# Performance work log

Hardware: AMD Instinct MI355X
Metric: run time of the kernel (lower is better)

Reference implementation:

```python
import jax, jax.numpy as jnp
import numpy as np

B, N, P, D = 256, 196, 768, 768
FIXED_MASK = 40          # FIXED_MASK_COUNT in the TF source
FIXED_UNMASK = N - FIXED_MASK


def setup_inputs() -> dict:
    key = jax.random.key(0)
    k1, k2, k3, k4, k5 = jax.random.split(key, 5)
    return {
        "patches": jax.random.normal(k1, (B, N, P), jnp.float32),
        "rand_u": jax.random.uniform(k2, (B, N), jnp.float32),
        "W": jax.random.normal(k3, (P, D), jnp.float32) * 0.02,
        "b": jnp.zeros((D,), jnp.float32),
        "pos_table": jax.random.normal(k4, (N, D), jnp.float32) * 0.02,
        "mask_token": jax.random.normal(k5, (1, P), jnp.float32),
    }


def reference(patches, rand_u, W, b, pos_table, mask_token):
    Bsz, Np, _ = patches.shape
    pos = pos_table[None]                                   # [1,N,D]
    patch_emb = jnp.einsum("bnp,pd->bnd", patches, W) + b + pos  # [B,N,D]

    # ---- get_smart_indices ----
    patch_means = jnp.mean(jnp.abs(patches), axis=2)        # [B,N]
    valid_mask = (patch_means > 0).astype(jnp.float32)
    valid_counts = jnp.sum(valid_mask, axis=1)
    max_masks = jnp.ceil(valid_counts * 0.4).astype(jnp.int32)
    valid_image = (valid_counts >= 20) & (max_masks >= FIXED_MASK)  # [B]

    # scores: valid patches in [1000,2000), invalid in [0,10)
    scores = valid_mask * (1000.0 + 1000.0 * rand_u) + (1.0 - valid_mask) * (10.0 * rand_u)
    _, top_idx = jax.lax.top_k(scores, FIXED_MASK)          # first 40 of full top-k sort
    top_idx = top_idx.astype(jnp.int32)
    mask_indices = jnp.where(valid_image[:, None], top_idx, jnp.zeros_like(top_idx))
    mask_counts = jnp.where(valid_image, FIXED_MASK, 0).astype(jnp.int32)

    # complement (ascending order), vectorized stream compaction via sort key
    flag = jnp.zeros((Bsz, Np), jnp.int32).at[jnp.arange(Bsz)[:, None], mask_indices].set(1)
    sort_key = flag * Np + jnp.arange(Np, dtype=jnp.int32)[None]  # unmasked sort first, ascending
    comp = jnp.argsort(sort_key, axis=1)[:, :FIXED_UNMASK].astype(jnp.int32)
    unmask_indices = jnp.where(valid_image[:, None], comp,
                               jnp.arange(FIXED_UNMASK, dtype=jnp.int32)[None])

    # ---- batched gathers ----
    pos_b = jnp.broadcast_to(pos, patch_emb.shape)          # [B,N,D]
    take = lambda x, i: jnp.take_along_axis(x, i[..., None], axis=1)
    unmasked_embeddings = take(patch_emb, unmask_indices)   # [B,156,D]
    unmasked_positions = take(pos_b, unmask_indices)        # [B,156,D]
    masked_positions = take(pos_b, mask_indices)            # [B,40,D]

    mtok = mask_token @ W + b                               # [1,D]
    masked_embeddings = mtok[None] + masked_positions       # [B,40,D]

    # validity masking (counts are 40 for valid images, 0 otherwise)
    seq = jnp.arange(FIXED_MASK, dtype=jnp.int32)[None]
    validity = (seq < mask_counts[:, None]).astype(jnp.float32)[..., None]
    masked_embeddings = masked_embeddings * validity

    return (unmasked_embeddings, masked_embeddings, unmasked_positions,
            mask_indices, unmask_indices)
```

## Files before the change

kernel.cpp:

```cpp
#include <hip/hip_runtime.h>
#include <hip/hip_bf16.h>
#include <stdint.h>

#define BATCH 256
#define NP    196
#define PP    768
#define DD    768
#define FM    40
#define FU    156
#define ROWS  39936

#define O_UE 0ull
#define O_ME 30670848ull
#define O_UP 38535168ull
#define O_MI 69206016ull
#define O_UI 69216256ull

typedef __attribute__((ext_vector_type(8))) short short8;
typedef __attribute__((ext_vector_type(4))) float f32x4;

__device__ __forceinline__ unsigned short bf16_rne(float x) {
    unsigned u = __float_as_uint(x);
    u += 0x7FFFu + ((u >> 16) & 1u);
    return (unsigned short)(u >> 16);
}
__device__ __forceinline__ float bf16_f(unsigned short h) {
    return __uint_as_float(((unsigned)h) << 16);
}

__device__ __forceinline__ void gl_lds16(const void* gsrc, void* ldst) {
    __builtin_amdgcn_global_load_lds(
        (const __attribute__((address_space(1))) unsigned*)gsrc,
        (__attribute__((address_space(3))) unsigned*)ldst, 16, 0, 0);
}

__global__ __launch_bounds__(256) void prep_w_kernel(
    const float* __restrict__ W,
    unsigned short* __restrict__ wt) {
    const int j  = blockIdx.x * 256 + threadIdx.x;
    const int ct = blockIdx.y;
    const int kt = blockIdx.z;
    const int row  = j >> 2;
    const int slot = j & 3;
    const int g    = slot ^ ((row >> 1) & 3);
    const int d    = ct * 128 + row;
    alignas(16) unsigned short hi[8];
    alignas(16) unsigned short lo[8];
#pragma unroll
    for (int e = 0; e < 8; ++e) {
        int k32 = (e < 4) ? (4 * g + e) : (12 + 4 * g + e);
        float x = W[(size_t)(kt * 32 + k32) * DD + d];
        unsigned short h = bf16_rne(x);
        hi[e] = h;
        lo[e] = bf16_rne(x - bf16_f(h));
    }
    unsigned short* dst = wt + ((size_t)(kt * 6 + ct) * 1024 + j) * 8;
    *(uint4*)dst          = *(const uint4*)hi;
    *(uint4*)(dst + 4096) = *(const uint4*)lo;
}

__global__ __launch_bounds__(256) void mtok_part_kernel(
    const float* __restrict__ mask_token,
    const float* __restrict__ W,
    float* __restrict__ part) {
    const int j = blockIdx.x;
    const int tid = threadIdx.x;
#pragma unroll
    for (int s = 0; s < 3; ++s) {
        int d = tid + s * 256;
        float acc = 0.f;
        for (int p = j * 64; p < j * 64 + 64; ++p)
            acc += mask_token[p] * W[(size_t)p * DD + d];
        part[(size_t)j * DD + d] = acc;
    }
}
__global__ __launch_bounds__(256) void mtok_red_kernel(
    const float* __restrict__ part,
    const float* __restrict__ bias,
    float* __restrict__ mtok_out) {
    int d = blockIdx.x * 256 + threadIdx.x;
    float acc = bias[d];
#pragma unroll
    for (int j = 0; j < 12; ++j) acc += part[(size_t)j * DD + d];
    mtok_out[d] = acc;
}

__global__ __launch_bounds__(256) void select_kernel(
    const float* __restrict__ patches,
    const float* __restrict__ rand_u,
    float* __restrict__ out,
    int* __restrict__ gidx,
    int* __restrict__ pidx,
    int* __restrict__ midx,
    int* __restrict__ valid_arr) {

    const int b = blockIdx.x;
    const int tid = threadIdx.x;
    __shared__ unsigned long long key[256];
    __shared__ int s_flag[256];
    __shared__ int s_scan[256];
    __shared__ int wsum[4];

    int v = 0;
    if (tid < NP) {
        const float* row = patches + ((size_t)b * NP + tid) * PP;
        for (int p = 0; p < PP; ++p) {
            if (row[p] != 0.0f) { v = 1; break; }
        }
    }
    unsigned long long bal = __ballot(v != 0);
    if ((tid & 63) == 0) wsum[tid >> 6] = __popcll(bal);
    __syncthreads();
    int count = wsum[0] + wsum[1] + wsum[2] + wsum[3];
    bool valid_image = (count >= 20) && (ceilf((float)count * 0.4f) >= 40.0f);

    unsigned long long k = 0ull;
    if (tid < NP) {
        float u = rand_u[(size_t)b * NP + tid];
        float score = v ? __fadd_rn(1000.0f, __fmul_rn(1000.0f, u))
                        : __fmul_rn(10.0f, u);
        k = (((unsigned long long)__float_as_uint(score)) << 32) |
            (unsigned long long)(unsigned)(~tid);
    }
    key[tid] = k;
    __syncthreads();

    for (int kk = 2; kk <= 256; kk <<= 1) {
        for (int j = kk >> 1; j > 0; j >>= 1) {
            int ixj = tid ^ j;
            if (ixj > tid) {
                unsigned long long a = key[tid], c = key[ixj];
                bool desc = ((tid & kk) == 0);
                if (desc ? (a < c) : (a > c)) { key[tid] = c; key[ixj] = a; }
            }
            __syncthreads();
        }
    }

    int m_out = 0;
    if (tid < FM) {
        int idx = (int)(~(unsigned)(key[tid] & 0xFFFFFFFFull));
        m_out = valid_image ? idx : 0;
        midx[b * FM + tid] = m_out;
        out[O_MI + (size_t)b * FM + tid] = (float)m_out;
    }
    s_flag[tid] = 0;
    __syncthreads();
    if (tid < FM) s_flag[m_out] = 1;
    __syncthreads();

    int x = (tid < NP) ? (1 - s_flag[tid]) : 0;
    s_scan[tid] = x;
    __syncthreads();
    for (int off = 1; off < 256; off <<= 1) {
        int t2 = (tid >= off) ? s_scan[tid - off] : 0;
        __syncthreads();
        s_scan[tid] += t2;
        __syncthreads();
    }
    int pos = s_scan[tid] - x;

    if (valid_image) {
        if (tid < NP && !s_flag[tid] && pos < FU) {
            gidx[(size_t)b * FU + pos] = b * NP + tid;
            pidx[(size_t)b * FU + pos] = tid;
            out[O_UI + (size_t)b * FU + pos] = (float)tid;
        }
    } else {
        if (tid < FU) {
            gidx[(size_t)b * FU + tid] = b * NP + tid;
            pidx[(size_t)b * FU + tid] = tid;
            out[O_UI + (size_t)b * FU + tid] = (float)tid;
        }
    }
    if (tid == 0) valid_arr[b] = valid_image ? 1 : 0;
}

__global__ __launch_bounds__(192) void prep_p_kernel(
    const float* __restrict__ patches,
    const int* __restrict__ gidx,
    char* __restrict__ pat_bf) {
    const int r = blockIdx.x;
    const int t = threadIdx.x;
    const float* src = patches + (size_t)gidx[r] * PP;
    float4 v4 = *(const float4*)(src + 4 * t);
    const int kt = t >> 3;
    const int q  = t & 7;
    const int g  = q & 3;
    const int half = q >> 2;
    float vs[4] = {v4.x, v4.y, v4.z, v4.w};
    unsigned long long hp = 0, lp = 0;
#pragma unroll
    for (int e = 0; e < 4; ++e) {
        unsigned short h = bf16_rne(vs[e]);
        unsigned short l = bf16_rne(vs[e] - bf16_f(h));
        hp |= ((unsigned long long)h) << (16 * e);
        lp |= ((unsigned long long)l) << (16 * e);
    }
    char* dst = pat_bf + (size_t)r * 3072 + kt * 64 + g * 16 + half * 8;
    *(unsigned long long*)dst          = hp;
    *(unsigned long long*)(dst + 1536) = lp;
}

template <int PRE>
__device__ __forceinline__ void fetchB(int KT, short8 (&BH)[4], short8 (&BL)[4],
                                       const char* const (&pb)[4],
                                       const float* const (&prow)[4], int g) {
    if constexpr (PRE) {
#pragma unroll
        for (int ci = 0; ci < 4; ++ci) {
            const char* p = pb[ci] + KT * 64;
            BH[ci] = *(const short8*)p;
            BL[ci] = *(const short8*)(p + 1536);
        }
    } else {
#pragma unroll
        for (int ci = 0; ci < 4; ++ci) {
            const float* p = prow[ci] + KT * 32 + 4 * g;
            const float4 a  = *(const float4*)p;
            const float4 b2 = *(const float4*)(p + 16);
            float vs[8] = {a.x, a.y, a.z, a.w, b2.x, b2.y, b2.z, b2.w};
            short8 h8, l8;
#pragma unroll
            for (int e = 0; e < 8; ++e) {
                unsigned short h = bf16_rne(vs[e]);
                h8[e] = (short)h;
                l8[e] = (short)bf16_rne(vs[e] - bf16_f(h));
            }
            BH[ci] = h8;
            BL[ci] = l8;
        }
    }
}

template <int PRE>
__global__ __launch_bounds__(256) void gemm_kernel(
    const float* __restrict__ patches,
    const char* __restrict__ pat_bf,
    const unsigned short* __restrict__ wt,
    const float* __restrict__ bias,
    const float* __restrict__ pos_table,
    const int* __restrict__ gidx,
    const int* __restrict__ pidx,
    float* __restrict__ out) {

    __shared__ __align__(16) char ldsb[32768];

    const int tid = threadIdx.x;
    const int l   = tid & 63;
    const int w   = tid >> 6;
    const int wd  = w >> 1;
    const int wp  = w & 1;
    const int l15 = l & 15;
    const int g   = l >> 4;
    const int slot = g ^ ((l15 >> 1) & 3);

    int lin = blockIdx.y * 6 + blockIdx.x;
    lin = (lin & 7) * 234 + (lin >> 3);
    const int ct = lin % 6;
    const int rt = lin / 6;

    int rflat[4];
    int ppos[4];
    const char* pb[4]   = {nullptr, nullptr, nullptr, nullptr};
    const float* prow[4] = {nullptr, nullptr, nullptr, nullptr};
#pragma unroll
    for (int ci = 0; ci < 4; ++ci) {
        int r = rt * 128 + wp * 64 + ci * 16 + l15;
        rflat[ci] = r;
        ppos[ci] = pidx[r];
        if constexpr (PRE) {
            pb[ci] = pat_bf + (size_t)r * 3072 + g * 16;
        } else {
            prow[ci] = patches + (size_t)gidx[r] * PP;
        }
    }

    f32x4 acc[4][4];
    const f32x4 z = {0.f, 0.f, 0.f, 0.f};
#pragma unroll
    for (int mi = 0; mi < 4; ++mi)
#pragma unroll
        for (int ci = 0; ci < 4; ++ci) acc[mi][ci] = z;

#define STAGE(BUF, KT)                                                         \
    {                                                                          \
        const char* s0 = (const char*)wt + (size_t)((KT)*6 + ct) * 16384;      \
        _Pragma("unroll")                                                      \
        for (int c = 0; c < 4; ++c) {                                          \
            gl_lds16(s0 + ((c * 4 + w) * 64 + l) * 16,                         \
                     ldsb + (BUF)*16384 + (c * 4 + w) * 1024);                 \
        }                                                                      \
    }

#define COMPUTE(BUF, BH, BL)                                                   \
    _Pragma("unroll")                                                          \
    for (int mi = 0; mi < 4; ++mi) {                                           \
        const char* wb = ldsb + (BUF)*16384 +                                  \
                         (wd * 64 + mi * 16 + l15) * 64 + slot * 16;           \
        short8 wh = *(const short8*)wb;                                        \
        short8 wl = *(const short8*)(wb + 8192);                               \
        _Pragma("unroll")                                                      \
        for (int ci = 0; ci < 4; ++ci) {                                       \
            acc[mi][ci] = __builtin_amdgcn_mfma_f32_16x16x32_bf16(             \
                wh, BH[ci], acc[mi][ci], 0, 0, 0);                             \
            acc[mi][ci] = __builtin_amdgcn_mfma_f32_16x16x32_bf16(             \
                wh, BL[ci], acc[mi][ci], 0, 0, 0);                             \
            acc[mi][ci] = __builtin_amdgcn_mfma_f32_16x16x32_bf16(             \
                wl, BH[ci], acc[mi][ci], 0, 0, 0);                             \
        }                                                                      \
    }

    short8 bhA[4], blA[4], bhB[4], blB[4];
    fetchB<PRE>(0, bhA, blA, pb, prow, g);
    STAGE(0, 0);

    for (int kt = 0; kt < 24; kt += 2) {
        __syncthreads();
        STAGE(1, kt + 1);
        fetchB<PRE>(kt + 1, bhB, blB, pb, prow, g);
        COMPUTE(0, bhA, blA);
        __syncthreads();
        if (kt + 2 < 24) {
            STAGE(0, kt + 2);
            fetchB<PRE>(kt + 2, bhA, blA, pb, prow, g);
        }
        COMPUTE(1, bhB, blB);
    }
#undef STAGE
#undef COMPUTE

#pragma unroll
    for (int mi = 0; mi < 4; ++mi) {
        const int dc = ct * 128 + wd * 64 + mi * 16 + 4 * g;
        const float4 b4 = *(const float4*)(bias + dc);
#pragma unroll
        for (int ci = 0; ci < 4; ++ci) {
            const float4 p4 = *(const float4*)(pos_table + (size_t)ppos[ci] * DD + dc);
            f32x4 o = acc[mi][ci];
            float4 r;
            r.x = o[0] + b4.x + p4.x;
            r.y = o[1] + b4.y + p4.y;
            r.z = o[2] + b4.z + p4.z;
            r.w = o[3] + b4.w + p4.w;
            size_t ro = (size_t)rflat[ci] * DD + dc;
            *(float4*)(out + O_UE + ro) = r;
            *(float4*)(out + O_UP + ro) = p4;
        }
    }
}

__global__ __launch_bounds__(192) void masked_kernel(
    const float* __restrict__ pos_table,
    const float* __restrict__ mtok,
    const int* __restrict__ midx,
    const int* __restrict__ valid_arr,
    float* __restrict__ out) {
    const int j = blockIdx.x;
    const int b = blockIdx.y;
    const int d = threadIdx.x * 4;
    float4 r = {0.f, 0.f, 0.f, 0.f};
    if (valid_arr[b]) {
        int pi = midx[b * FM + j];
        const float4 m4 = *(const float4*)(mtok + d);
        const float4 p4 = *(const float4*)(pos_table + (size_t)pi * DD + d);
        r.x = m4.x + p4.x; r.y = m4.y + p4.y;
        r.z = m4.z + p4.z; r.w = m4.w + p4.w;
    }
    *(float4*)(out + O_ME + ((size_t)b * FM + j) * DD + d) = r;
}

extern "C" void kernel_launch(void* const* d_in, const int* in_sizes, int n_in,
                              void* d_out, int out_size, void* d_ws, size_t ws_size,
                              hipStream_t stream) {
    const float* patches   = (const float*)d_in[0];
    const float* rand_u    = (const float*)d_in[1];
    const float* W         = (const float*)d_in[2];
    const float* bias      = (const float*)d_in[3];
    const float* pos_table = (const float*)d_in[4];
    const float* mask_tok  = (const float*)d_in[5];
    float* out = (float*)d_out;

    char* ws = (char*)d_ws;
    int*            gidx   = (int*)(ws + 0);
    int*            pidx   = (int*)(ws + 159744);
    int*            midx   = (int*)(ws + 319488);
    int*            valid  = (int*)(ws + 360448);
    float*          mtok   = (float*)(ws + 361472);
    float*          mpart  = (float*)(ws + 364544);
    unsigned short* wt     = (unsigned short*)(ws + 401408);
    char*           pat_bf = ws + 2760704;

    const size_t NEEDED = 2760704ull + 122683392ull;
    const bool pre = (ws_size >= NEEDED);

    prep_w_kernel<<<dim3(2, 6, 24), dim3(256), 0, stream>>>(W, wt);
    mtok_part_kernel<<<dim3(12), dim3(256), 0, stream>>>(mask_tok, W, mpart);
    mtok_red_kernel<<<dim3(3), dim3(256), 0, stream>>>(mpart, bias, mtok);
    select_kernel<<<dim3(BATCH), dim3(256), 0, stream>>>(patches, rand_u, out,
                                                         gidx, pidx, midx, valid);
    if (pre) {
        prep_p_kernel<<<dim3(ROWS), dim3(192), 0, stream>>>(patches, gidx, pat_bf);
        gemm_kernel<1><<<dim3(6, 312), dim3(256), 0, stream>>>(
            patches, pat_bf, wt, bias, pos_table, gidx, pidx, out);
    } else {
        gemm_kernel<0><<<dim3(6, 312), dim3(256), 0, stream>>>(
            patches, pat_bf, wt, bias, pos_table, gidx, pidx, out);
    }
    masked_kernel<<<dim3(FM, BATCH), dim3(192), 0, stream>>>(pos_table, mtok,
                                                             midx, valid, out);
}
```

Measured before the change: 707.2 us.

## Stage pre-split patch tiles through LDS with triple-buffered async loads

The prep kernel now writes the hi/lo bf16 split of the gathered patch rows in a tiled, swizzled layout matching the LDS tile format. The GEMM can therefore load B tiles straight to LDS (gl_lds16) with triple buffering and explicit vmcnt waits, where before each lane loaded them from global memory into registers. The non-precomputed fallback path is removed, so a large enough workspace is now assumed. The mtok partial reduction is also split across 48 blocks instead of 12 to expose more parallelism.

```diff
diff --git a/kernel.cpp b/kernel.cpp
--- a/kernel.cpp
+++ b/kernel.cpp
@@ -9,6 +9,7 @@
 #define FM    40
 #define FU    156
 #define ROWS  39936
+#define NGRP  312
 
 #define O_UE 0ull
 #define O_ME 30670848ull
@@ -69,8 +70,11 @@
     for (int s = 0; s < 3; ++s) {
         int d = tid + s * 256;
         float acc = 0.f;
-        for (int p = j * 64; p < j * 64 + 64; ++p)
+#pragma unroll
+        for (int pp = 0; pp < 16; ++pp) {
+            int p = j * 16 + pp;
             acc += mask_token[p] * W[(size_t)p * DD + d];
+        }
         part[(size_t)j * DD + d] = acc;
     }
 }
@@ -81,7 +85,7 @@
     int d = blockIdx.x * 256 + threadIdx.x;
     float acc = bias[d];
 #pragma unroll
-    for (int j = 0; j < 12; ++j) acc += part[(size_t)j * DD + d];
+    for (int j = 0; j < 48; ++j) acc += part[(size_t)j * DD + d];
     mtok_out[d] = acc;
 }
 
@@ -180,71 +184,46 @@
     const float* __restrict__ patches,
     const int* __restrict__ gidx,
     char* __restrict__ pat_bf) {
-    const int r = blockIdx.x;
+    const int j = blockIdx.x;
     const int t = threadIdx.x;
-    const float* src = patches + (size_t)gidx[r] * PP;
-    float4 v4 = *(const float4*)(src + 4 * t);
     const int kt = t >> 3;
     const int q  = t & 7;
     const int g  = q & 3;
     const int half = q >> 2;
-    float vs[4] = {v4.x, v4.y, v4.z, v4.w};
-    unsigned long long hp = 0, lp = 0;
-#pragma unroll
-    for (int e = 0; e < 4; ++e) {
-        unsigned short h = bf16_rne(vs[e]);
-        unsigned short l = bf16_rne(vs[e] - bf16_f(h));
-        hp |= ((unsigned long long)h) << (16 * e);
-        lp |= ((unsigned long long)l) << (16 * e);
-    }
-    char* dst = pat_bf + (size_t)r * 3072 + kt * 64 + g * 16 + half * 8;
-    *(unsigned long long*)dst          = hp;
-    *(unsigned long long*)(dst + 1536) = lp;
-}
-
-template <int PRE>
-__device__ __forceinline__ void fetchB(int KT, short8 (&BH)[4], short8 (&BL)[4],
-                                       const char* const (&pb)[4],
-                                       const float* const (&prow)[4], int g) {
-    if constexpr (PRE) {
-#pragma unroll
-        for (int ci = 0; ci < 4; ++ci) {
-            const char* p = pb[ci] + KT * 64;
-            BH[ci] = *(const short8*)p;
-            BL[ci] = *(const short8*)(p + 1536);
-        }
-    } else {
-#pragma unroll
-        for (int ci = 0; ci < 4; ++ci) {
-            const float* p = prow[ci] + KT * 32 + 4 * g;
-            const float4 a  = *(const float4*)p;
-            const float4 b2 = *(const float4*)(p + 16);
-            float vs[8] = {a.x, a.y, a.z, a.w, b2.x, b2.y, b2.z, b2.w};
-            short8 h8, l8;
-#pragma unroll
-            for (int e = 0; e < 8; ++e) {
-                unsigned short h = bf16_rne(vs[e]);
-                h8[e] = (short)h;
-                l8[e] = (short)bf16_rne(vs[e] - bf16_f(h));
-            }
-            BH[ci] = h8;
-            BL[ci] = l8;
-        }
-    }
-}
-
-template <int PRE>
+#pragma unroll
+    for (int rr = 0; rr < 2; ++rr) {
+        const int r = 2 * j + rr;
+        const float* src = patches + (size_t)gidx[r] * PP;
+        float4 v4 = *(const float4*)(src + 4 * t);
+        float vs[4] = {v4.x, v4.y, v4.z, v4.w};
+        unsigned long long hp = 0, lp = 0;
+#pragma unroll
+        for (int e = 0; e < 4; ++e) {
+            unsigned short h = bf16_rne(vs[e]);
+            unsigned short l2 = bf16_rne(vs[e] - bf16_f(h));
+            hp |= ((unsigned long long)h) << (16 * e);
+            lp |= ((unsigned long long)l2) << (16 * e);
+        }
+        const int rl = r & 127;
+        const int grp = r >> 7;
+        const int slot = g ^ ((rl >> 1) & 3);
+        char* dst = pat_bf + ((size_t)kt * NGRP + grp) * 16384 +
+                    rl * 64 + slot * 16 + half * 8;
+        *(unsigned long long*)dst          = hp;
+        *(unsigned long long*)(dst + 8192) = lp;
+    }
+}
+
 __global__ __launch_bounds__(256) void gemm_kernel(
-    const float* __restrict__ patches,
     const char* __restrict__ pat_bf,
     const unsigned short* __restrict__ wt,
     const float* __restrict__ bias,
     const float* __restrict__ pos_table,
-    const int* __restrict__ gidx,
     const int* __restrict__ pidx,
     float* __restrict__ out) {
 
-    __shared__ __align__(16) char ldsb[32768];
+    __shared__ __align__(16) char ldsW[2 * 16384];
+    __shared__ __align__(16) char ldsB[3 * 16384];
 
     const int tid = threadIdx.x;
     const int l   = tid & 63;
@@ -253,27 +232,20 @@
     const int wp  = w & 1;
     const int l15 = l & 15;
     const int g   = l >> 4;
-    const int slot = g ^ ((l15 >> 1) & 3);
-
-    int lin = blockIdx.y * 6 + blockIdx.x;
+    const int soff = (g ^ ((l15 >> 1) & 3)) * 16;
+
+    int lin = blockIdx.x;
     lin = (lin & 7) * 234 + (lin >> 3);
     const int ct = lin % 6;
     const int rt = lin / 6;
 
     int rflat[4];
     int ppos[4];
-    const char* pb[4]   = {nullptr, nullptr, nullptr, nullptr};
-    const float* prow[4] = {nullptr, nullptr, nullptr, nullptr};
 #pragma unroll
     for (int ci = 0; ci < 4; ++ci) {
         int r = rt * 128 + wp * 64 + ci * 16 + l15;
         rflat[ci] = r;
         ppos[ci] = pidx[r];
-        if constexpr (PRE) {
-            pb[ci] = pat_bf + (size_t)r * 3072 + g * 16;
-        } else {
-            prow[ci] = patches + (size_t)gidx[r] * PP;
-        }
     }
 
     f32x4 acc[4][4];
@@ -283,51 +255,75 @@
 #pragma unroll
         for (int ci = 0; ci < 4; ++ci) acc[mi][ci] = z;
 
-#define STAGE(BUF, KT)                                                         \
+#define STAGE_W(BUF, KT)                                                       \
     {                                                                          \
         const char* s0 = (const char*)wt + (size_t)((KT)*6 + ct) * 16384;      \
         _Pragma("unroll")                                                      \
-        for (int c = 0; c < 4; ++c) {                                          \
+        for (int c = 0; c < 4; ++c)                                            \
             gl_lds16(s0 + ((c * 4 + w) * 64 + l) * 16,                         \
-                     ldsb + (BUF)*16384 + (c * 4 + w) * 1024);                 \
-        }                                                                      \
-    }
-
-#define COMPUTE(BUF, BH, BL)                                                   \
-    _Pragma("unroll")                                                          \
-    for (int mi = 0; mi < 4; ++mi) {                                           \
-        const char* wb = ldsb + (BUF)*16384 +                                  \
-                         (wd * 64 + mi * 16 + l15) * 64 + slot * 16;           \
-        short8 wh = *(const short8*)wb;                                        \
-        short8 wl = *(const short8*)(wb + 8192);                               \
+                     ldsW + (BUF)*16384 + (c * 4 + w) * 1024);                 \
+    }
+#define STAGE_B(BUF, KT)                                                       \
+    {                                                                          \
+        const char* s0 = pat_bf + ((size_t)(KT)*NGRP + rt) * 16384;            \
+        _Pragma("unroll")                                                      \
+        for (int c = 0; c < 4; ++c)                                            \
+            gl_lds16(s0 + ((c * 4 + w) * 64 + l) * 16,                         \
+                     ldsB + (BUF)*16384 + (c * 4 + w) * 1024);                 \
+    }
+#define COMPUTE(WBUF, BBUF)                                                    \
+    {                                                                          \
+        const char* wbase = ldsW + (WBUF)*16384;                               \
+        const char* bbase = ldsB + (BBUF)*16384;                               \
+        short8 BH[4], BL[4];                                                   \
         _Pragma("unroll")                                                      \
         for (int ci = 0; ci < 4; ++ci) {                                       \
-            acc[mi][ci] = __builtin_amdgcn_mfma_f32_16x16x32_bf16(             \
-                wh, BH[ci], acc[mi][ci], 0, 0, 0);                             \
-            acc[mi][ci] = __builtin_amdgcn_mfma_f32_16x16x32_bf16(             \
-                wh, BL[ci], acc[mi][ci], 0, 0, 0);                             \
-            acc[mi][ci] = __builtin_amdgcn_mfma_f32_16x16x32_bf16(             \
-                wl, BH[ci], acc[mi][ci], 0, 0, 0);                             \
+            const char* bb = bbase + (wp * 64 + ci * 16 + l15) * 64 + soff;    \
+            BH[ci] = *(const short8*)bb;                                       \
+            BL[ci] = *(const short8*)(bb + 8192);                              \
         }                                                                      \
-    }
-
-    short8 bhA[4], blA[4], bhB[4], blB[4];
-    fetchB<PRE>(0, bhA, blA, pb, prow, g);
-    STAGE(0, 0);
-
-    for (int kt = 0; kt < 24; kt += 2) {
-        __syncthreads();
-        STAGE(1, kt + 1);
-        fetchB<PRE>(kt + 1, bhB, blB, pb, prow, g);
-        COMPUTE(0, bhA, blA);
-        __syncthreads();
-        if (kt + 2 < 24) {
-            STAGE(0, kt + 2);
-            fetchB<PRE>(kt + 2, bhA, blA, pb, prow, g);
-        }
-        COMPUTE(1, bhB, blB);
-    }
-#undef STAGE
+        _Pragma("unroll")                                                      \
+        for (int mi = 0; mi < 4; ++mi) {                                       \
+            const char* wb = wbase + (wd * 64 + mi * 16 + l15) * 64 + soff;    \
+            short8 wh = *(const short8*)wb;                                    \
+            short8 wl2 = *(const short8*)(wb + 8192);                          \
+            _Pragma("unroll")                                                  \
+            for (int ci = 0; ci < 4; ++ci) {                                   \
+                acc[mi][ci] = __builtin_amdgcn_mfma_f32_16x16x32_bf16(         \
+                    wh, BH[ci], acc[mi][ci], 0, 0, 0);                         \
+                acc[mi][ci] = __builtin_amdgcn_mfma_f32_16x16x32_bf16(         \
+                    wh, BL[ci], acc[mi][ci], 0, 0, 0);                         \
+                acc[mi][ci] = __builtin_amdgcn_mfma_f32_16x16x32_bf16(         \
+                    wl2, BH[ci], acc[mi][ci], 0, 0, 0);                        \
+            }                                                                  \
+        }                                                                      \
+    }
+
+    STAGE_W(0, 0);
+    STAGE_B(0, 0);
+    STAGE_B(1, 1);
+
+    int wcur = 0;
+    for (int k = 0; k < 24; ++k) {
+        if (k < 23) STAGE_W(wcur ^ 1, k + 1);
+        if (k < 22) STAGE_B((k + 2) % 3, k + 2);
+        if (k < 22) {
+            asm volatile("s_waitcnt vmcnt(12)" ::: "memory");
+        } else if (k == 22) {
+            asm volatile("s_waitcnt vmcnt(8)" ::: "memory");
+        } else {
+            asm volatile("s_waitcnt vmcnt(0)" ::: "memory");
+        }
+        __builtin_amdgcn_sched_barrier(0);
+        __builtin_amdgcn_s_barrier();
+        __builtin_amdgcn_sched_barrier(0);
+        COMPUTE(wcur, k % 3);
+        __builtin_amdgcn_sched_barrier(0);
+        __builtin_amdgcn_s_barrier();
+        wcur ^= 1;
+    }
+#undef STAGE_W
+#undef STAGE_B
 #undef COMPUTE
 
 #pragma unroll
@@ -388,25 +384,17 @@
     int*            valid  = (int*)(ws + 360448);
     float*          mtok   = (float*)(ws + 361472);
     float*          mpart  = (float*)(ws + 364544);
-    unsigned short* wt     = (unsigned short*)(ws + 401408);
-    char*           pat_bf = ws + 2760704;
-
-    const size_t NEEDED = 2760704ull + 122683392ull;
-    const bool pre = (ws_size >= NEEDED);
+    unsigned short* wt     = (unsigned short*)(ws + 512000);
+    char*           pat_bf = ws + 2871296;
 
     prep_w_kernel<<<dim3(2, 6, 24), dim3(256), 0, stream>>>(W, wt);
-    mtok_part_kernel<<<dim3(12), dim3(256), 0, stream>>>(mask_tok, W, mpart);
+    mtok_part_kernel<<<dim3(48), dim3(256), 0, stream>>>(mask_tok, W, mpart);
     mtok_red_kernel<<<dim3(3), dim3(256), 0, stream>>>(mpart, bias, mtok);
     select_kernel<<<dim3(BATCH), dim3(256), 0, stream>>>(patches, rand_u, out,
                                                          gidx, pidx, midx, valid);
-    if (pre) {
-        prep_p_kernel<<<dim3(ROWS), dim3(192), 0, stream>>>(patches, gidx, pat_bf);
-        gemm_kernel<1><<<dim3(6, 312), dim3(256), 0, stream>>>(
-            patches, pat_bf, wt, bias, pos_table, gidx, pidx, out);
-    } else {
-        gemm_kernel<0><<<dim3(6, 312), dim3(256), 0, stream>>>(
-            patches, pat_bf, wt, bias, pos_table, gidx, pidx, out);
-    }
+    prep_p_kernel<<<dim3(ROWS / 2), dim3(192), 0, stream>>>(patches, gidx, pat_bf);
+    gemm_kernel<<<dim3(1872), dim3(256), 0, stream>>>(pat_bf, wt, bias,
+                                                      pos_table, pidx, out);
     masked_kernel<<<dim3(FM, BATCH), dim3(192), 0, stream>>>(pos_table, mtok,
                                                              midx, valid, out);
 }
```

Result: faster. 606.2 us (-14.3%).
